# Kernel optimization log

Hardware: AMD Instinct MI355X
Metric: run time of the kernel (lower is better)

Reference implementation:

```python
import jax, jax.numpy as jnp
import numpy as np
import math

DIM = 4096
N_HEADS = 4
KV_RANK = 1024
HEAD_DIM = DIM // N_HEADS  # 1024, must equal KV_RANK for the source matmul to work
THETA = 10000.0


def rope(x):
    # x: [B, S, H, D]; interleaved even/odd RoPE, D taken from tensor (as in source)
    B, S, H, D = x.shape
    freqs = 1.0 / (THETA ** (jnp.arange(0, D, 2, dtype=jnp.float32) / D))  # [D/2]
    angles = jnp.arange(S, dtype=jnp.float32)[:, None] * freqs[None, :]    # [S, D/2]
    cos = jnp.cos(angles)[None, :, None, :]  # [1,S,1,D/2]
    sin = jnp.sin(angles)[None, :, None, :]
    x1 = x[..., 0::2]
    x2 = x[..., 1::2]
    xr = cos * x1 - sin * x2
    yr = cos * x2 + sin * x1
    return jnp.stack([xr, yr], axis=-1).reshape(B, S, H, D)


def setup_inputs() -> dict:
    key = jax.random.key(0)
    ks = jax.random.split(key, 6)
    B, S = 4, 4096
    x = jax.random.normal(ks[0], (B, S, DIM), dtype=jnp.float32)
    mask = jax.random.randint(ks[1], (B, S, 1, 1), 0, 2, dtype=jnp.int32)
    sc = 0.02
    Wq = jax.random.normal(ks[2], (DIM, DIM), dtype=jnp.float32) * sc
    Wk = jax.random.normal(ks[3], (KV_RANK, DIM), dtype=jnp.float32) * sc
    Wv = jax.random.normal(ks[4], (KV_RANK, DIM), dtype=jnp.float32) * sc
    Wo = jax.random.normal(ks[5], (DIM, DIM), dtype=jnp.float32) * sc
    return {"x": x, "Wq": Wq, "Wk": Wk, "Wv": Wv, "Wo": Wo, "mask": mask}


def reference(x, Wq, Wk, Wv, Wo, mask):
    B, S, _ = x.shape
    q = jnp.einsum('bsd,ed->bse', x, Wq).reshape(B, S, N_HEADS, HEAD_DIM)
    k = jnp.einsum('bsd,ed->bse', x, Wk).reshape(B, S, 1, KV_RANK)
    v = jnp.einsum('bsd,ed->bse', x, Wv).reshape(B, S, 1, KV_RANK)
    q = rope(q)
    k = rope(k)
    # batched matmul over (B,S): [B,S,H,D] @ [B,S,D,1] -> [B,S,H,1]
    scores = jnp.einsum('bshd,bsjd->bshj', q, k) / math.sqrt(HEAD_DIM)
    scores = jnp.where(mask == 0, jnp.float32(-1e9), scores)
    attn = jax.nn.softmax(scores, axis=-1)  # size-1 axis, as in source
    out = jnp.einsum('bshj,bsjd->bshd', attn, v).reshape(B, S, -1)
    return jnp.einsum('bse,de->bsd', out, Wo)
```

## Files before the change

### kernel.cpp

```cpp
#include <hip/hip_runtime.h>

typedef unsigned short u16;
typedef __bf16 bf16x8 __attribute__((ext_vector_type(8)));
typedef float f32x4 __attribute__((ext_vector_type(4)));

__device__ __forceinline__ u16 f2bf(float f) {
  unsigned u = __float_as_uint(f);
  u += 0x7FFF + ((u >> 16) & 1);
  return (u16)(u >> 16);
}

__device__ __forceinline__ unsigned pack2(float lo, float hi) {
  return (unsigned)f2bf(lo) | ((unsigned)f2bf(hi) << 16);
}

__device__ __forceinline__ void gload_lds16(const void* g, void* l) {
  __builtin_amdgcn_global_load_lds(
      (const __attribute__((address_space(1))) void*)g,
      (__attribute__((address_space(3))) void*)l,
      16, 0, 0);
}

__device__ __forceinline__ int swzb(int lin) {
  return lin ^ (((lin >> 7) & 7) << 4);
}

__global__ void prep_all(const float4* __restrict__ x, const float* __restrict__ Wv,
                         const float* __restrict__ Wo, uint4* __restrict__ xb,
                         uint4* __restrict__ Wvb, uint4* __restrict__ Wofb) {
  const int nx = (16384 * 4096) / 8;
  const int nw = (1024 * 4096) / 8;
  int i = blockIdx.x * blockDim.x + threadIdx.x;
  const int stride = gridDim.x * blockDim.x;
  for (; i < nx + 2 * nw; i += stride) {
    if (i < nx) {
      float4 a = x[(size_t)i * 2], b = x[(size_t)i * 2 + 1];
      xb[i] = make_uint4(pack2(a.x, a.y), pack2(a.z, a.w),
                         pack2(b.x, b.y), pack2(b.z, b.w));
    } else if (i < nx + nw) {
      int j = i - nx;
      const float4* p = (const float4*)Wv + (size_t)j * 2;
      float4 a = p[0], b = p[1];
      Wvb[j] = make_uint4(pack2(a.x, a.y), pack2(a.z, a.w),
                          pack2(b.x, b.y), pack2(b.z, b.w));
    } else {
      int j = i - nx - nw;
      int row = j >> 7;
      int c = (j & 127) * 8;
      float4 s0 = {0.f, 0.f, 0.f, 0.f}, s1 = {0.f, 0.f, 0.f, 0.f};
#pragma unroll
      for (int h = 0; h < 4; ++h) {
        const float4* p = (const float4*)(Wo + (size_t)row * 4096 + h * 1024 + c);
        float4 a = p[0], b = p[1];
        s0.x += a.x; s0.y += a.y; s0.z += a.z; s0.w += a.w;
        s1.x += b.x; s1.y += b.y; s1.z += b.z; s1.w += b.w;
      }
      Wofb[j] = make_uint4(pack2(s0.x, s0.y), pack2(s0.z, s0.w),
                           pack2(s1.x, s1.y), pack2(s1.z, s1.w));
    }
  }
}

__device__ __forceinline__ void stage_half(const char* g, int ldb, char* ldsTile,
                                           int regionBase, int tid) {
#pragma unroll
  for (int j = 0; j < 2; ++j) {
    const int un = regionBase + j * 8192 + (tid >> 6) * 1024;
    const int l  = swzb(un + (tid & 63) * 16);
    gload_lds16(g + (size_t)(l >> 7) * (size_t)ldb + (l & 127), ldsTile + un);
  }
}

__device__ __forceinline__ void stage_Ahalf(const char* g, int ldb, char* ldsA,
                                            int which, int tid) {
#pragma unroll
  for (int j = 0; j < 2; ++j) {
    const int un = (which ? 8192 : 0) + j * 16384 + (tid >> 6) * 1024;
    const int l  = swzb(un + (tid & 63) * 16);
    gload_lds16(g + (size_t)(l >> 7) * (size_t)ldb + (l & 127), ldsA + un);
  }
}

template<int P, class Stage>
__device__ __forceinline__ void do_phase(f32x4 (&acc)[8][4], const bf16x8 (&bfr)[4][2],
                                         const char* sA, const int wrow, const int lm,
                                         const int hi16, const int axor, Stage&& stage) {
  bf16x8 afr[2][2];
#pragma unroll
  for (int m2 = 0; m2 < 2; ++m2)
#pragma unroll
    for (int kk = 0; kk < 2; ++kk) {
      const int row = wrow * 128 + (P * 2 + m2) * 16 + lm;
      afr[m2][kk] = *(const bf16x8*)(sA + ((row * 128 + kk * 64 + hi16) ^ axor));
    }
  stage();
  __builtin_amdgcn_s_barrier();
  asm volatile("s_waitcnt lgkmcnt(0)" ::: "memory");
  __builtin_amdgcn_s_setprio(1);
#pragma unroll
  for (int kk = 0; kk < 2; ++kk)
#pragma unroll
    for (int m2 = 0; m2 < 2; ++m2)
#pragma unroll
      for (int ni = 0; ni < 4; ++ni)
        acc[P * 2 + m2][ni] = __builtin_amdgcn_mfma_f32_16x16x32_bf16(
            afr[m2][kk], bfr[ni][kk], acc[P * 2 + m2][ni], 0, 0, 0);
  __builtin_amdgcn_s_setprio(0);
}

template<bool OUT_BF16, int REPS>
__global__ __launch_bounds__(512, 2) void gemm256(
    const u16* __restrict__ A, const u16* __restrict__ B, void* __restrict__ Cv,
    int M, int N, int K) {
  extern __shared__ char smem[];

  const int tid  = threadIdx.x;
  const int lane = tid & 63;
  const int wave = tid >> 6;
  const int wrow = wave >> 2;
  const int wcol = wave & 3;
  const int lm   = lane & 15;
  const int hi16 = (lane >> 4) * 16;
  const int axor = (lm & 7) << 4;

  const int swzid = (blockIdx.x & 7) * 32 + (blockIdx.x >> 3);
  const int nbn = N >> 8;
  const int ldb = K * 2;
  const int nt  = K >> 6;

#pragma unroll 1
  for (int rep = 0; rep < REPS; ++rep) {
    const int id = rep * 256 + swzid;
    const int bm = id / nbn, bn = id % nbn;
    const char* Ab = (const char*)A + (size_t)bm * 256 * (size_t)ldb;
    const char* Bb = (const char*)B + (size_t)bn * 256 * (size_t)ldb;

    f32x4 acc[8][4];
#pragma unroll
    for (int m = 0; m < 8; ++m)
#pragma unroll
      for (int n = 0; n < 4; ++n) acc[m][n] = {0.f, 0.f, 0.f, 0.f};

    {
      char* s0A = smem;            char* s0B = smem + 32768;
      char* s1A = smem + 65536;    char* s1B = s1A + 32768;
      stage_half (Bb, ldb, s0B, 0, tid);
      stage_half (Bb, ldb, s0B, 16384, tid);
      stage_Ahalf(Ab, ldb, s0A, 0, tid);
      stage_Ahalf(Ab, ldb, s0A, 1, tid);
      if (nt > 1) {
        stage_half (Bb + 128, ldb, s1B, 0, tid);
        stage_half (Bb + 128, ldb, s1B, 16384, tid);
        stage_Ahalf(Ab + 128, ldb, s1A, 0, tid);
        asm volatile("s_waitcnt vmcnt(6)" ::: "memory");
      } else {
        asm volatile("s_waitcnt vmcnt(0)" ::: "memory");
      }
      __builtin_amdgcn_s_barrier();
    }

#pragma unroll 1
    for (int t = 0; t < nt; ++t) {
      char* sA = smem + (t & 1) * 65536;
      char* sB = sA + 32768;
      char* oA = smem + ((t & 1) ^ 1) * 65536;
      const char* Ag1 = Ab + (size_t)(t + 1) * 128;
      const char* Ag2 = Ab + (size_t)(t + 2) * 128;
      const char* Bg2 = Bb + (size_t)(t + 2) * 128;

      bf16x8 bfr[4][2];
#pragma unroll
      for (int ni = 0; ni < 4; ++ni)
#pragma unroll
        for (int kk = 0; kk < 2; ++kk) {
          const int row = wcol * 64 + ni * 16 + lm;
          bfr[ni][kk] = *(const bf16x8*)(sB + ((row * 128 + kk * 64 + hi16) ^ axor));
        }

      do_phase<0>(acc, bfr, sA, wrow, lm, hi16, axor,
                  [&] { if (t + 1 < nt) stage_Ahalf(Ag1, ldb, oA, 1, tid); });
      __builtin_amdgcn_s_barrier();
      do_phase<1>(acc, bfr, sA, wrow, lm, hi16, axor,
                  [&] { if (t + 2 < nt) stage_half(Bg2, ldb, sB, 0, tid); });
      __builtin_amdgcn_s_barrier();
      do_phase<2>(acc, bfr, sA, wrow, lm, hi16, axor,
                  [&] { if (t + 2 < nt) stage_half(Bg2, ldb, sB, 16384, tid); });
      __builtin_amdgcn_s_barrier();
      do_phase<3>(acc, bfr, sA, wrow, lm, hi16, axor,
                  [&] { if (t + 2 < nt) stage_Ahalf(Ag2, ldb, sA, 0, tid); });
      if (t + 2 < nt)      asm volatile("s_waitcnt vmcnt(6)" ::: "memory");
      else if (t + 1 < nt) asm volatile("s_waitcnt vmcnt(0)" ::: "memory");
      __builtin_amdgcn_s_barrier();
    }

    const int lr = (lane >> 4) * 4;
#pragma unroll
    for (int m = 0; m < 8; ++m) {
      const long row0 = (long)bm * 256 + wrow * 128 + m * 16 + lr;
#pragma unroll
      for (int ni = 0; ni < 4; ++ni) {
        const long col = (long)bn * 256 + wcol * 64 + ni * 16 + lm;
#pragma unroll
        for (int r = 0; r < 4; ++r) {
          const long idx = (row0 + r) * N + col;
          if constexpr (OUT_BF16) ((u16*)Cv)[idx] = f2bf(acc[m][ni][r]);
          else                    ((float*)Cv)[idx] = acc[m][ni][r];
        }
      }
    }
  }
}

extern "C" void kernel_launch(void* const* d_in, const int* in_sizes, int n_in,
                              void* d_out, int out_size, void* d_ws, size_t ws_size,
                              hipStream_t stream) {
  const float* x  = (const float*)d_in[0];
  const float* Wv = (const float*)d_in[3];
  const float* Wo = (const float*)d_in[4];

  const int M = 16384;
  const int D = 4096;
  const int R = 1024;

  u16* vb   = (u16*)d_ws;
  u16* Wvb  = vb + (size_t)M * R;
  u16* Wofb = Wvb + (size_t)R * D;
  u16* xb   = (u16*)d_out;

  (void)hipFuncSetAttribute((const void*)gemm256<true, 1>,
                            hipFuncAttributeMaxDynamicSharedMemorySize, 131072);
  (void)hipFuncSetAttribute((const void*)gemm256<false, 4>,
                            hipFuncAttributeMaxDynamicSharedMemorySize, 131072);

  prep_all<<<dim3(2048), dim3(256), 0, stream>>>((const float4*)x, Wv, Wo,
                                                 (uint4*)xb, (uint4*)Wvb, (uint4*)Wofb);
  gemm256<true, 1><<<dim3(256), dim3(512), 131072, stream>>>(xb, Wvb, vb, M, R, D);
  gemm256<false, 4><<<dim3(256), dim3(512), 131072, stream>>>(vb, Wofb, (float*)d_out, M, D, R);
}
```

Measured before the change: 363.8 us.

## Double-buffer LDS fragments in registers to prefetch one phase ahead

The GEMM main loop is restructured so A and B fragment reads from LDS are issued one MFMA phase ahead into alternating register buffers. This removes the explicit lgkmcnt(0) stall before each phase's MFMAs. The loop is unrolled by two so register and LDS buffers can swap roles. The cost is extra VGPRs (second A and B fragment sets) under a 512-thread, 2-block launch bound, which may cause spills or lower occupancy. The next tile's fragments are read after a per-thread vmcnt wait but before a barrier, which may race with other waves' global-to-LDS loads.

```diff
diff --git a/kernel.cpp b/kernel.cpp
--- a/kernel.cpp
+++ b/kernel.cpp
@@ -81,21 +81,29 @@
   }
 }
 
-template<int P, class Stage>
-__device__ __forceinline__ void do_phase(f32x4 (&acc)[8][4], const bf16x8 (&bfr)[4][2],
-                                         const char* sA, const int wrow, const int lm,
-                                         const int hi16, const int axor, Stage&& stage) {
-  bf16x8 afr[2][2];
+__device__ __forceinline__ void load_afr(bf16x8 (&a)[2][2], const char* sA, int rowbase,
+                                         int lm, int hi16, int axor) {
 #pragma unroll
   for (int m2 = 0; m2 < 2; ++m2)
 #pragma unroll
-    for (int kk = 0; kk < 2; ++kk) {
-      const int row = wrow * 128 + (P * 2 + m2) * 16 + lm;
-      afr[m2][kk] = *(const bf16x8*)(sA + ((row * 128 + kk * 64 + hi16) ^ axor));
-    }
-  stage();
-  __builtin_amdgcn_s_barrier();
-  asm volatile("s_waitcnt lgkmcnt(0)" ::: "memory");
+    for (int kk = 0; kk < 2; ++kk)
+      a[m2][kk] = *(const bf16x8*)(
+          sA + ((((rowbase + m2 * 16 + lm) * 128) + kk * 64 + hi16) ^ axor));
+}
+
+__device__ __forceinline__ void load_bfr(bf16x8 (&b)[4][2], const char* sB, int wcol,
+                                         int lm, int hi16, int axor) {
+#pragma unroll
+  for (int ni = 0; ni < 4; ++ni)
+#pragma unroll
+    for (int kk = 0; kk < 2; ++kk)
+      b[ni][kk] = *(const bf16x8*)(
+          sB + ((((wcol * 64 + ni * 16 + lm) * 128) + kk * 64 + hi16) ^ axor));
+}
+
+template<int P>
+__device__ __forceinline__ void phase_mfma(f32x4 (&acc)[8][4], const bf16x8 (&af)[2][2],
+                                           const bf16x8 (&bf)[4][2]) {
   __builtin_amdgcn_s_setprio(1);
 #pragma unroll
   for (int kk = 0; kk < 2; ++kk)
@@ -104,8 +112,42 @@
 #pragma unroll
       for (int ni = 0; ni < 4; ++ni)
         acc[P * 2 + m2][ni] = __builtin_amdgcn_mfma_f32_16x16x32_bf16(
-            afr[m2][kk], bfr[ni][kk], acc[P * 2 + m2][ni], 0, 0, 0);
+            af[m2][kk], bf[ni][kk], acc[P * 2 + m2][ni], 0, 0, 0);
   __builtin_amdgcn_s_setprio(0);
+}
+
+__device__ __forceinline__ void tile_body(
+    f32x4 (&acc)[8][4], bf16x8 (&afrA)[2][2], bf16x8 (&afrB)[2][2],
+    const bf16x8 (&bfrU)[4][2], bf16x8 (&bfrN)[4][2],
+    char* sA, char* sB, char* oA, char* oB,
+    const char* Ag1, const char* Ag2, const char* Bg2,
+    bool c1, bool c2, int tid, int wrow, int wcol, int lm, int hi16, int axor, int ldb) {
+  const int rb = wrow * 128;
+  load_afr(afrB, sA, rb + 32, lm, hi16, axor);
+  if (c1) stage_Ahalf(Ag1, ldb, oA, 1, tid);
+  __builtin_amdgcn_s_barrier();
+  phase_mfma<0>(acc, afrA, bfrU);
+  __builtin_amdgcn_s_barrier();
+  load_afr(afrA, sA, rb + 64, lm, hi16, axor);
+  if (c2) stage_half(Bg2, ldb, sB, 0, tid);
+  __builtin_amdgcn_s_barrier();
+  phase_mfma<1>(acc, afrB, bfrU);
+  __builtin_amdgcn_s_barrier();
+  load_afr(afrB, sA, rb + 96, lm, hi16, axor);
+  if (c2) stage_half(Bg2, ldb, sB, 16384, tid);
+  __builtin_amdgcn_s_barrier();
+  phase_mfma<2>(acc, afrA, bfrU);
+  __builtin_amdgcn_s_barrier();
+  if (c2) stage_Ahalf(Ag2, ldb, sA, 0, tid);
+  if (c2)      asm volatile("s_waitcnt vmcnt(6)" ::: "memory");
+  else if (c1) asm volatile("s_waitcnt vmcnt(0)" ::: "memory");
+  if (c1) {
+    load_bfr(bfrN, oB, wcol, lm, hi16, axor);
+    load_afr(afrA, oA, rb, lm, hi16, axor);
+  }
+  __builtin_amdgcn_s_barrier();
+  phase_mfma<3>(acc, afrB, bfrU);
+  __builtin_amdgcn_s_barrier();
 }
 
 template<bool OUT_BF16, int REPS>
@@ -140,6 +182,8 @@
     for (int m = 0; m < 8; ++m)
 #pragma unroll
       for (int n = 0; n < 4; ++n) acc[m][n] = {0.f, 0.f, 0.f, 0.f};
+
+    bf16x8 afrA[2][2], afrB[2][2], bfrA[4][2], bfrB[4][2];
 
     {
       char* s0A = smem;            char* s0B = smem + 32768;
@@ -157,40 +201,22 @@
         asm volatile("s_waitcnt vmcnt(0)" ::: "memory");
       }
       __builtin_amdgcn_s_barrier();
+      load_bfr(bfrA, s0B, wcol, lm, hi16, axor);
+      load_afr(afrA, s0A, wrow * 128, lm, hi16, axor);
     }
 
 #pragma unroll 1
-    for (int t = 0; t < nt; ++t) {
-      char* sA = smem + (t & 1) * 65536;
-      char* sB = sA + 32768;
-      char* oA = smem + ((t & 1) ^ 1) * 65536;
-      const char* Ag1 = Ab + (size_t)(t + 1) * 128;
-      const char* Ag2 = Ab + (size_t)(t + 2) * 128;
-      const char* Bg2 = Bb + (size_t)(t + 2) * 128;
-
-      bf16x8 bfr[4][2];
-#pragma unroll
-      for (int ni = 0; ni < 4; ++ni)
-#pragma unroll
-        for (int kk = 0; kk < 2; ++kk) {
-          const int row = wcol * 64 + ni * 16 + lm;
-          bfr[ni][kk] = *(const bf16x8*)(sB + ((row * 128 + kk * 64 + hi16) ^ axor));
-        }
-
-      do_phase<0>(acc, bfr, sA, wrow, lm, hi16, axor,
-                  [&] { if (t + 1 < nt) stage_Ahalf(Ag1, ldb, oA, 1, tid); });
-      __builtin_amdgcn_s_barrier();
-      do_phase<1>(acc, bfr, sA, wrow, lm, hi16, axor,
-                  [&] { if (t + 2 < nt) stage_half(Bg2, ldb, sB, 0, tid); });
-      __builtin_amdgcn_s_barrier();
-      do_phase<2>(acc, bfr, sA, wrow, lm, hi16, axor,
-                  [&] { if (t + 2 < nt) stage_half(Bg2, ldb, sB, 16384, tid); });
-      __builtin_amdgcn_s_barrier();
-      do_phase<3>(acc, bfr, sA, wrow, lm, hi16, axor,
-                  [&] { if (t + 2 < nt) stage_Ahalf(Ag2, ldb, sA, 0, tid); });
-      if (t + 2 < nt)      asm volatile("s_waitcnt vmcnt(6)" ::: "memory");
-      else if (t + 1 < nt) asm volatile("s_waitcnt vmcnt(0)" ::: "memory");
-      __builtin_amdgcn_s_barrier();
+    for (int t = 0; t < nt; t += 2) {
+      tile_body(acc, afrA, afrB, bfrA, bfrB,
+                smem, smem + 32768, smem + 65536, smem + 98304,
+                Ab + (size_t)(t + 1) * 128, Ab + (size_t)(t + 2) * 128,
+                Bb + (size_t)(t + 2) * 128,
+                t + 1 < nt, t + 2 < nt, tid, wrow, wcol, lm, hi16, axor, ldb);
+      tile_body(acc, afrA, afrB, bfrB, bfrA,
+                smem + 65536, smem + 98304, smem, smem + 32768,
+                Ab + (size_t)(t + 2) * 128, Ab + (size_t)(t + 3) * 128,
+                Bb + (size_t)(t + 3) * 128,
+                t + 2 < nt, t + 3 < nt, tid, wrow, wcol, lm, hi16, axor, ldb);
     }
 
     const int lr = (lane >> 4) * 4;
```

Result: slower. 1.426 ms (+291.9%).

## Chain second GEMM tiles per block so prefetch crosses tile boundaries

Applied to the files above, without the earlier changes.

The second GEMM now assigns each block a fixed row panel and four consecutive column tiles. The software pipeline keeps prefetching the next tile's B data and wraps the A loads across reps, which removes the prologue and drain stall between tiles. The cost is more complex address logic, and each block is tied to one A row panel, which changes L2 reuse patterns.

```diff
diff --git a/kernel.cpp b/kernel.cpp
--- a/kernel.cpp
+++ b/kernel.cpp
@@ -108,7 +108,7 @@
   __builtin_amdgcn_s_setprio(0);
 }
 
-template<bool OUT_BF16, int REPS>
+template<bool OUT_BF16, int REPS, bool CHAIN>
 __global__ __launch_bounds__(512, 2) void gemm256(
     const u16* __restrict__ A, const u16* __restrict__ B, void* __restrict__ Cv,
     int M, int N, int K) {
@@ -130,8 +130,9 @@
 
 #pragma unroll 1
   for (int rep = 0; rep < REPS; ++rep) {
-    const int id = rep * 256 + swzid;
-    const int bm = id / nbn, bn = id % nbn;
+    int bm, bn;
+    if constexpr (CHAIN) { bm = swzid >> 2; bn = (swzid & 3) * 4 + rep; }
+    else { const int id = rep * 256 + swzid; bm = id / nbn; bn = id % nbn; }
     const char* Ab = (const char*)A + (size_t)bm * 256 * (size_t)ldb;
     const char* Bb = (const char*)B + (size_t)bn * 256 * (size_t)ldb;
 
@@ -141,7 +142,7 @@
 #pragma unroll
       for (int n = 0; n < 4; ++n) acc[m][n] = {0.f, 0.f, 0.f, 0.f};
 
-    {
+    if (!CHAIN || rep == 0) {
       char* s0A = smem;            char* s0B = smem + 32768;
       char* s1A = smem + 65536;    char* s1B = s1A + 32768;
       stage_half (Bb, ldb, s0B, 0, tid);
@@ -164,9 +165,24 @@
       char* sA = smem + (t & 1) * 65536;
       char* sB = sA + 32768;
       char* oA = smem + ((t & 1) ^ 1) * 65536;
-      const char* Ag1 = Ab + (size_t)(t + 1) * 128;
-      const char* Ag2 = Ab + (size_t)(t + 2) * 128;
-      const char* Bg2 = Bb + (size_t)(t + 2) * 128;
+
+      const char *Ag1, *Ag2, *Bg2;
+      bool c1, c2;
+      if constexpr (CHAIN) {
+        Ag1 = Ab + (size_t)(((t + 1) & (nt - 1)) * 128);
+        Ag2 = Ab + (size_t)(((t + 2) & (nt - 1)) * 128);
+        Bg2 = (t + 2 < nt) ? Bb + (size_t)(t + 2) * 128
+                           : Bb + (size_t)256 * (size_t)ldb + (size_t)(t + 2 - nt) * 128;
+        const bool lastrep = (rep == REPS - 1);
+        c1 = !lastrep || (t + 1 < nt);
+        c2 = !lastrep || (t + 2 < nt);
+      } else {
+        Ag1 = Ab + (size_t)(t + 1) * 128;
+        Ag2 = Ab + (size_t)(t + 2) * 128;
+        Bg2 = Bb + (size_t)(t + 2) * 128;
+        c1 = (t + 1 < nt);
+        c2 = (t + 2 < nt);
+      }
 
       bf16x8 bfr[4][2];
 #pragma unroll
@@ -178,18 +194,18 @@
         }
 
       do_phase<0>(acc, bfr, sA, wrow, lm, hi16, axor,
-                  [&] { if (t + 1 < nt) stage_Ahalf(Ag1, ldb, oA, 1, tid); });
+                  [&] { if (c1) stage_Ahalf(Ag1, ldb, oA, 1, tid); });
       __builtin_amdgcn_s_barrier();
       do_phase<1>(acc, bfr, sA, wrow, lm, hi16, axor,
-                  [&] { if (t + 2 < nt) stage_half(Bg2, ldb, sB, 0, tid); });
+                  [&] { if (c2) stage_half(Bg2, ldb, sB, 0, tid); });
       __builtin_amdgcn_s_barrier();
       do_phase<2>(acc, bfr, sA, wrow, lm, hi16, axor,
-                  [&] { if (t + 2 < nt) stage_half(Bg2, ldb, sB, 16384, tid); });
+                  [&] { if (c2) stage_half(Bg2, ldb, sB, 16384, tid); });
       __builtin_amdgcn_s_barrier();
       do_phase<3>(acc, bfr, sA, wrow, lm, hi16, axor,
-                  [&] { if (t + 2 < nt) stage_Ahalf(Ag2, ldb, sA, 0, tid); });
-      if (t + 2 < nt)      asm volatile("s_waitcnt vmcnt(6)" ::: "memory");
-      else if (t + 1 < nt) asm volatile("s_waitcnt vmcnt(0)" ::: "memory");
+                  [&] { if (c2) stage_Ahalf(Ag2, ldb, sA, 0, tid); });
+      if (c2)      asm volatile("s_waitcnt vmcnt(6)" ::: "memory");
+      else if (c1) asm volatile("s_waitcnt vmcnt(0)" ::: "memory");
       __builtin_amdgcn_s_barrier();
     }
 
@@ -227,13 +243,13 @@
   u16* Wofb = Wvb + (size_t)R * D;
   u16* xb   = (u16*)d_out;
 
-  (void)hipFuncSetAttribute((const void*)gemm256<true, 1>,
+  (void)hipFuncSetAttribute((const void*)gemm256<true, 1, false>,
                             hipFuncAttributeMaxDynamicSharedMemorySize, 131072);
-  (void)hipFuncSetAttribute((const void*)gemm256<false, 4>,
+  (void)hipFuncSetAttribute((const void*)gemm256<false, 4, true>,
                             hipFuncAttributeMaxDynamicSharedMemorySize, 131072);
 
   prep_all<<<dim3(2048), dim3(256), 0, stream>>>((const float4*)x, Wv, Wo,
                                                  (uint4*)xb, (uint4*)Wvb, (uint4*)Wofb);
-  gemm256<true, 1><<<dim3(256), dim3(512), 131072, stream>>>(xb, Wvb, vb, M, R, D);
-  gemm256<false, 4><<<dim3(256), dim3(512), 131072, stream>>>(vb, Wofb, (float*)d_out, M, D, R);
-}
+  gemm256<true, 1, false><<<dim3(256), dim3(512), 131072, stream>>>(xb, Wvb, vb, M, R, D);
+  gemm256<false, 4, true><<<dim3(256), dim3(512), 131072, stream>>>(vb, Wofb, (float*)d_out, M, D, R);
+}
```

Result: slower. 383.0 us (+5.3%).
